# Optimization experiments

Measured on AMD Instinct MI355X. Metric: run time of the kernel, lower is better.

Reference implementation:

```python
import jax, jax.numpy as jnp
import numpy as np

N, E, F_IN, H = 50000, 800000, 500, 96

def setup_inputs() -> dict:
    key = jax.random.key(0)
    ks = jax.random.split(key, 10)
    x = jax.random.normal(ks[0], (N, F_IN), dtype=jnp.float32)
    src = jax.random.randint(ks[1], (E,), 0, N, dtype=jnp.int32)
    dst = jax.random.randint(ks[2], (E,), 0, N, dtype=jnp.int32)
    perm = jax.random.permutation(ks[3], N).astype(jnp.int32)
    W1 = jax.random.normal(ks[4], (F_IN, H), dtype=jnp.float32) / np.sqrt(F_IN)
    b1 = jnp.zeros((H,), jnp.float32)
    a1 = jnp.full((H,), 0.25, jnp.float32)  # PReLU init
    W2 = jax.random.normal(ks[5], (H, H), dtype=jnp.float32) / np.sqrt(H)
    b2 = jnp.zeros((H,), jnp.float32)
    a2 = jnp.full((H,), 0.25, jnp.float32)
    Wm = jax.random.normal(ks[6], (H, H), dtype=jnp.float32) / np.sqrt(H)
    bm = jnp.zeros((H,), jnp.float32)
    return {"x": x, "src": src, "dst": dst, "perm": perm,
            "W1": W1, "b1": b1, "a1": a1, "W2": W2, "b2": b2, "a2": a2,
            "Wm": Wm, "bm": bm}

def reference(x, src, dst, perm, W1, b1, a1, W2, b2, a2, Wm, bm):
    n = x.shape[0]
    ones = jnp.ones_like(src, dtype=x.dtype)
    deg_out = jnp.clip(jax.ops.segment_sum(ones, src, num_segments=n), 1.0)
    deg_in = jnp.clip(jax.ops.segment_sum(ones, dst, num_segments=n), 1.0)
    norm_out = (deg_out ** -0.5)[:, None]  # [N,1]
    norm_in = (deg_in ** -0.5)[:, None]

    def gconv(h, W, b, a):
        # DGL GraphConv, norm='both': D_out^-1/2 -> W -> A -> D_in^-1/2 -> +b -> PReLU
        h = (h * norm_out) @ W                                  # [N,H]
        agg = jax.ops.segment_sum(h[src], dst, num_segments=n)  # SpMM via gather/scatter
        h = agg * norm_in + b
        return jnp.where(h >= 0, h, a * h)                      # PReLU

    def encode(feat):
        h = gconv(feat, W1, b1, a1)
        return gconv(h, W2, b2, a2)

    z1 = encode(x)
    z2 = encode(x[perm])  # corrupted view: permuted node features
    z1 = z1 @ Wm + bm
    z2 = z2 @ Wm + bm
    return jnp.concatenate([z1.sum(1), z2.sum(1)], axis=0)  # [2N]
```

## Files before the change

### kernel.cpp

```cpp
#include <hip/hip_runtime.h>

#define H96 96

typedef __attribute__((ext_vector_type(8))) short bf16x8_t;
typedef __attribute__((ext_vector_type(4))) float f32x4_t;
typedef __attribute__((ext_vector_type(8))) _Float16 half8_t;

#define NRANGE 8
#define NCHUNK 64

__global__ __launch_bounds__(256) void hist2_kernel(const int* __restrict__ src,
                                                    const int* __restrict__ dst,
                                                    unsigned short* __restrict__ parts,
                                                    int E, int RS, int ecpc) {
    extern __shared__ int h[];
    int r = blockIdx.x >> 6;
    int c = blockIdx.x & 63;
    int lo = r * RS;
    for (int i = threadIdx.x; i < 2 * RS; i += 256) h[i] = 0;
    __syncthreads();
    int e0 = c * ecpc;
    int e1 = min(e0 + ecpc, E);
    for (int base = e0 + threadIdx.x * 4; base < e1; base += 1024) {
        int cnt = min(4, e1 - base);
        if (cnt == 4) {
            int4 sv = *(const int4*)(src + base);
            int4 dv = *(const int4*)(dst + base);
            int a;
            a = sv.x - lo; if ((unsigned)a < (unsigned)RS) atomicAdd(&h[a], 1);
            a = sv.y - lo; if ((unsigned)a < (unsigned)RS) atomicAdd(&h[a], 1);
            a = sv.z - lo; if ((unsigned)a < (unsigned)RS) atomicAdd(&h[a], 1);
            a = sv.w - lo; if ((unsigned)a < (unsigned)RS) atomicAdd(&h[a], 1);
            a = dv.x - lo; if ((unsigned)a < (unsigned)RS) atomicAdd(&h[RS + a], 1);
            a = dv.y - lo; if ((unsigned)a < (unsigned)RS) atomicAdd(&h[RS + a], 1);
            a = dv.z - lo; if ((unsigned)a < (unsigned)RS) atomicAdd(&h[RS + a], 1);
            a = dv.w - lo; if ((unsigned)a < (unsigned)RS) atomicAdd(&h[RS + a], 1);
        } else {
            for (int k = 0; k < cnt; k++) {
                int a = src[base + k] - lo;
                if ((unsigned)a < (unsigned)RS) atomicAdd(&h[a], 1);
                a = dst[base + k] - lo;
                if ((unsigned)a < (unsigned)RS) atomicAdd(&h[RS + a], 1);
            }
        }
    }
    __syncthreads();
    unsigned short* po = parts + ((size_t)(r * 2 + 0) * NCHUNK + c) * RS;
    unsigned short* pi = parts + ((size_t)(r * 2 + 1) * NCHUNK + c) * RS;
    for (int i = threadIdx.x; i < RS; i += 256) {
        po[i] = (unsigned short)h[i];
        pi[i] = (unsigned short)h[RS + i];
    }
}

__global__ void degred_kernel(const unsigned short* __restrict__ parts,
                              const int* __restrict__ perm,
                              int* __restrict__ deg_in, int* __restrict__ iperm,
                              float* __restrict__ no, float* __restrict__ ni,
                              int N, int RS) {
    int i = blockIdx.x * 256 + threadIdx.x;
    if (i >= N) return;
    int r = i / RS, idx = i - r * RS;
    const unsigned short* po = parts + ((size_t)(r * 2 + 0) * NCHUNK) * RS + idx;
    const unsigned short* pi = parts + ((size_t)(r * 2 + 1) * NCHUNK) * RS + idx;
    int so = 0, si = 0;
#pragma unroll
    for (int c = 0; c < NCHUNK; c++) {
        so += po[(size_t)c * RS];
        si += pi[(size_t)c * RS];
    }
    deg_in[i] = si;
    no[i] = rsqrtf(fmaxf((float)so, 1.0f));
    ni[i] = rsqrtf(fmaxf((float)si, 1.0f));
    iperm[perm[i]] = i;
}

__global__ void scanA_kernel(const int* __restrict__ in, int* __restrict__ pre,
                             int* __restrict__ bsums, int n) {
    __shared__ int s[256];
    int i = blockIdx.x * 256 + threadIdx.x;
    int v = (i < n) ? in[i] : 0;
    s[threadIdx.x] = v;
    __syncthreads();
    for (int off = 1; off < 256; off <<= 1) {
        int t = (threadIdx.x >= off) ? s[threadIdx.x - off] : 0;
        __syncthreads();
        s[threadIdx.x] += t;
        __syncthreads();
    }
    if (i < n) pre[i] = s[threadIdx.x] - v;
    if (threadIdx.x == 255) bsums[blockIdx.x] = s[255];
}

__global__ void scanB_kernel(int* __restrict__ bsums, int nb) {
    __shared__ int s[256];
    int v = (threadIdx.x < nb) ? bsums[threadIdx.x] : 0;
    s[threadIdx.x] = v;
    __syncthreads();
    for (int off = 1; off < 256; off <<= 1) {
        int t = (threadIdx.x >= off) ? s[threadIdx.x - off] : 0;
        __syncthreads();
        s[threadIdx.x] += t;
        __syncthreads();
    }
    if (threadIdx.x < nb) bsums[threadIdx.x] = s[threadIdx.x] - v;
}

__global__ void rowfin_kernel(const int* __restrict__ pre, const int* __restrict__ bsums,
                              int* __restrict__ row_start, int* __restrict__ cursor,
                              int N, int E) {
    int i = blockIdx.x * 256 + threadIdx.x;
    if (i < N) {
        int v = pre[i] + bsums[blockIdx.x];
        row_start[i] = v;
        cursor[i] = v;
    }
    if (i == 0) row_start[N] = E;
}

__global__ void scatter_kernel(const int* __restrict__ src, const int* __restrict__ dst,
                               const float* __restrict__ norm_out,
                               int* __restrict__ cursor, int2* __restrict__ edge2, int E) {
    int e = blockIdx.x * 256 + threadIdx.x;
    if (e < E) {
        int d = dst[e];
        int s = src[e];
        int p = atomicAdd(cursor + d, 1);
        edge2[p] = make_int2(s, __float_as_int(norm_out[s]));
    }
}

__global__ void histblk_kernel(const int* __restrict__ deg, int* __restrict__ hb,
                               int N, int nb) {
    __shared__ int h[256];
    h[threadIdx.x] = 0;
    __syncthreads();
    int i = blockIdx.x * 256 + threadIdx.x;
    if (i < N) atomicAdd(&h[min(deg[i], 255)], 1);
    __syncthreads();
    hb[threadIdx.x * nb + blockIdx.x] = h[threadIdx.x];
}

__global__ void place2_kernel(const int* __restrict__ deg, const int* __restrict__ hpre,
                              const int* __restrict__ bsums, int* __restrict__ order,
                              int N, int nb) {
    __shared__ int cur[256];
    int idx = threadIdx.x * nb + blockIdx.x;
    cur[threadIdx.x] = hpre[idx] + bsums[idx >> 8];
    __syncthreads();
    int i = blockIdx.x * 256 + threadIdx.x;
    if (i < N) {
        int b = min(deg[i], 255);
        int p = atomicAdd(&cur[b], 1);
        order[p] = i;
    }
}

__device__ __forceinline__ void f2bf2(float v, unsigned short& h, unsigned short& l) {
    unsigned int b = __float_as_uint(v);
    unsigned short hh = (unsigned short)((b + 0x7FFFu + ((b >> 16) & 1u)) >> 16);
    float fh = __uint_as_float(((unsigned int)hh) << 16);
    float r = v - fh;
    unsigned int rb = __float_as_uint(r);
    unsigned short ll = (unsigned short)((rb + 0x7FFFu + ((rb >> 16) & 1u)) >> 16);
    h = hh; l = ll;
}

__device__ __forceinline__ void cvt8(const float f[8], bf16x8_t& ah, bf16x8_t& al) {
    union { unsigned int u[4]; bf16x8_t v; } H, L;
#pragma unroll
    for (int i = 0; i < 4; i++) {
        float v0 = f[2 * i], v1 = f[2 * i + 1];
        unsigned int b0 = __float_as_uint(v0);
        unsigned int b1 = __float_as_uint(v1);
        unsigned int m0 = b0 & 0xFFFF0000u;
        unsigned int m1 = b1 & 0xFFFF0000u;
        float r0 = v0 - __uint_as_float(m0);
        float r1 = v1 - __uint_as_float(m1);
        H.u[i] = (b0 >> 16) | m1;
        L.u[i] = (__float_as_uint(r0) >> 16) | (__float_as_uint(r1) & 0xFFFF0000u);
    }
    ah = H.v; al = L.v;
}

__global__ void weights_prep(const float* __restrict__ W1, const float* __restrict__ W2,
                             const float* __restrict__ Wm, const float* __restrict__ bm,
                             unsigned short* __restrict__ w1h, unsigned short* __restrict__ w1l,
                             unsigned short* __restrict__ w2h, unsigned short* __restrict__ w2l,
                             float* __restrict__ wsum, float* __restrict__ bsum,
                             int F, int KP1) {
    int idx = blockIdx.x * 256 + threadIdx.x;
    int z1 = 96 * KP1, z2 = z1 + 96 * 96;
    if (idx < z1) {
        int n = idx / KP1, k = idx - n * KP1;
        float v = (k < F) ? W1[(size_t)k * 96 + n] : 0.f;
        unsigned short h, l;
        f2bf2(v, h, l);
        w1h[idx] = h; w1l[idx] = l;
    } else if (idx < z2) {
        int t = idx - z1;
        int n = t / 96, k = t - n * 96;
        float v = W2[(size_t)k * 96 + n];
        unsigned short h, l;
        f2bf2(v, h, l);
        w2h[t] = h; w2l[t] = l;
    } else if (idx < z2 + 96) {
        int c = idx - z2;
        float s = 0.f;
        for (int j = 0; j < 96; j++) s += Wm[c * 96 + j];
        wsum[c] = s;
    } else if (idx == z2 + 96) {
        float s = 0.f;
        for (int j = 0; j < 96; j++) s += bm[j];
        bsum[0] = s;
    }
}

#define GBM 64
#define GBK 32

__device__ __forceinline__ void gload_lds16(const void* g, void* l) {
    __builtin_amdgcn_global_load_lds(
        (const __attribute__((address_space(1))) unsigned int*)g,
        (__attribute__((address_space(3))) unsigned int*)l, 16, 0, 0);
}

__global__ __launch_bounds__(256, 6) void gemm_mfma(const void* __restrict__ Av,
                                                    const unsigned short* __restrict__ Bth,
                                                    const unsigned short* __restrict__ Btl,
                                                    _Float16* __restrict__ C16,
                                                    const int* __restrict__ ipermArr,
                                                    int M, int K, int KP) {
    __shared__ alignas(16) unsigned short Bs[2][2][96][4][8];
    int tid = threadIdx.x;
    int wid = tid >> 6, lane = tid & 63;
    int q = lane >> 4, mn = lane & 15;
    int row0 = blockIdx.x * GBM + wid * 16;
    int arow = min(row0 + mn, M - 1);
    int nk = (K + GBK - 1) / GBK;

    const float* A32 = (const float*)Av;

    const unsigned short* gsrc[3];
    int lbase[3];
#pragma unroll
    for (int i = 0; i < 3; i++) {
        int c = wid * 192 + i * 64 + lane;
        int part = (c >= 384) ? 1 : 0;
        int rem = c - part * 384;
        int row = rem >> 2, slot = rem & 3;
        int kc = slot ^ ((row >> 1) & 3);
        gsrc[i] = (part ? Btl : Bth) + (size_t)row * KP + kc * 8;
        lbase[i] = (wid * 192 + i * 64) * 8;
    }

    auto stage = [&](int t, int buf) {
#pragma unroll
        for (int i = 0; i < 3; i++)
            gload_lds16(gsrc[i] + (size_t)t * GBK, &Bs[buf][0][0][0][0] + lbase[i]);
    };

    auto loadA = [&](int t, float* f) {
        int gk = t * GBK + q * 8;
        if (gk + 8 <= K) {
            float4 v0 = *(const float4*)(A32 + (size_t)arow * K + gk);
            float4 v1 = *(const float4*)(A32 + (size_t)arow * K + gk + 4);
            f[0] = v0.x; f[1] = v0.y; f[2] = v0.z; f[3] = v0.w;
            f[4] = v1.x; f[5] = v1.y; f[6] = v1.z; f[7] = v1.w;
        } else {
#pragma unroll
            for (int c = 0; c < 8; c++)
                f[c] = (gk + c < K) ? A32[(size_t)arow * K + gk + c] : 0.f;
        }
    };

    f32x4_t acc[6] = {};
    float f[8], fn[8];

    stage(0, 0);
    loadA(0, f);

    int slotR = q ^ ((mn >> 1) & 3);

    for (int t = 0; t < nk; t++) {
        int tn = (t + 1 < nk) ? t + 1 : nk - 1;
        stage(tn, (t + 1) & 1);
        loadA(tn, fn);
        asm volatile("s_waitcnt vmcnt(5)" ::: "memory");
        __builtin_amdgcn_sched_barrier(0);
        __builtin_amdgcn_s_barrier();

        bf16x8_t ah, al;
        cvt8(f, ah, al);

        const unsigned short* bp = &Bs[t & 1][0][0][0][0] + mn * 32 + slotR * 8;
#pragma unroll
        for (int ct = 0; ct < 6; ct++) {
            bf16x8_t bh = *(const bf16x8_t*)(bp + ct * 512);
            bf16x8_t bl = *(const bf16x8_t*)(bp + 3072 + ct * 512);
            acc[ct] = __builtin_amdgcn_mfma_f32_16x16x32_bf16(ah, bh, acc[ct], 0, 0, 0);
            acc[ct] = __builtin_amdgcn_mfma_f32_16x16x32_bf16(ah, bl, acc[ct], 0, 0, 0);
            acc[ct] = __builtin_amdgcn_mfma_f32_16x16x32_bf16(al, bh, acc[ct], 0, 0, 0);
        }
        asm volatile("s_waitcnt lgkmcnt(0)" ::: "memory");
        __builtin_amdgcn_sched_barrier(0);
        __builtin_amdgcn_s_barrier();

#pragma unroll
        for (int c = 0; c < 8; c++) f[c] = fn[c];
    }

    asm volatile("s_waitcnt vmcnt(0)" ::: "memory");
    __builtin_amdgcn_sched_barrier(0);

#pragma unroll
    for (int reg = 0; reg < 4; reg++) {
        int gr = row0 + q * 4 + reg;
        if (gr < M) {
            int ip = ipermArr[gr];
#pragma unroll
            for (int ct = 0; ct < 6; ct++) {
                _Float16 v = (_Float16)acc[ct][reg];
                C16[(size_t)gr * 192 + ct * 16 + mn] = v;
                C16[(size_t)ip * 192 + 96 + ct * 16 + mn] = v;
            }
        }
    }
}

__global__ __launch_bounds__(256, 4) void gemm_small(const _Float16* __restrict__ A16,
                                                     const unsigned short* __restrict__ Bth,
                                                     const unsigned short* __restrict__ Btl,
                                                     _Float16* __restrict__ C16,
                                                     int M) {
    __shared__ alignas(16) unsigned short Bs[3][2][96][4][8];
    const int K = 96;
    int tid = threadIdx.x;
    int wid = tid >> 6, lane = tid & 63;
    int q = lane >> 4, mn = lane & 15;
    int row0 = blockIdx.x * GBM + wid * 16;
    int arow = min(row0 + mn, M - 1);

    const unsigned short* gsrc[3];
    int lbase[3];
#pragma unroll
    for (int i = 0; i < 3; i++) {
        int c = wid * 192 + i * 64 + lane;
        int part = (c >= 384) ? 1 : 0;
        int rem = c - part * 384;
        int row = rem >> 2, slot = rem & 3;
        int kc = slot ^ ((row >> 1) & 3);
        gsrc[i] = (part ? Btl : Bth) + (size_t)row * K + kc * 8;
        lbase[i] = (wid * 192 + i * 64) * 8;
    }

#pragma unroll
    for (int t = 0; t < 3; t++)
#pragma unroll
        for (int i = 0; i < 3; i++)
            gload_lds16(gsrc[i] + (size_t)t * GBK, &Bs[t][0][0][0][0] + lbase[i]);

    uint4 ra0 = *(const uint4*)(A16 + (size_t)arow * K + 0 * GBK + q * 8);
    uint4 ra1 = *(const uint4*)(A16 + (size_t)arow * K + 1 * GBK + q * 8);
    uint4 ra2 = *(const uint4*)(A16 + (size_t)arow * K + 2 * GBK + q * 8);

    asm volatile("s_waitcnt vmcnt(0)" ::: "memory");
    __builtin_amdgcn_sched_barrier(0);
    __builtin_amdgcn_s_barrier();

    f32x4_t acc[6] = {};
    int slotR = q ^ ((mn >> 1) & 3);

    auto step = [&](int t, const uint4& raw) {
        float f[8];
        const _Float16* hp = (const _Float16*)&raw;
#pragma unroll
        for (int c = 0; c < 8; c++) f[c] = (float)hp[c];
        bf16x8_t ah, al;
        cvt8(f, ah, al);
        const unsigned short* bp = &Bs[t][0][0][0][0] + mn * 32 + slotR * 8;
#pragma unroll
        for (int ct = 0; ct < 6; ct++) {
            bf16x8_t bh = *(const bf16x8_t*)(bp + ct * 512);
            bf16x8_t bl = *(const bf16x8_t*)(bp + 3072 + ct * 512);
            acc[ct] = __builtin_amdgcn_mfma_f32_16x16x32_bf16(ah, bh, acc[ct], 0, 0, 0);
            acc[ct] = __builtin_amdgcn_mfma_f32_16x16x32_bf16(ah, bl, acc[ct], 0, 0, 0);
            acc[ct] = __builtin_amdgcn_mfma_f32_16x16x32_bf16(al, bh, acc[ct], 0, 0, 0);
        }
    };

    step(0, ra0);
    step(1, ra1);
    step(2, ra2);

#pragma unroll
    for (int reg = 0; reg < 4; reg++) {
        int gr = row0 + q * 4 + reg;
        if (gr < M) {
#pragma unroll
            for (int ct = 0; ct < 6; ct++)
                C16[(size_t)gr * H96 + ct * 16 + mn] = (_Float16)acc[ct][reg];
        }
    }
}

__device__ __forceinline__ void fmah8(float4& a, float4& b, float s, half8_t v) {
    a.x = fmaf(s, (float)v[0], a.x); a.y = fmaf(s, (float)v[1], a.y);
    a.z = fmaf(s, (float)v[2], a.z); a.w = fmaf(s, (float)v[3], a.w);
    b.x = fmaf(s, (float)v[4], b.x); b.y = fmaf(s, (float)v[5], b.y);
    b.z = fmaf(s, (float)v[6], b.z); b.w = fmaf(s, (float)v[7], b.w);
}

__device__ __forceinline__ float4 prelu4(float4 acc, float ni, float4 b, float4 a) {
    float4 h;
    h.x = fmaf(acc.x, ni, b.x); h.x = (h.x >= 0.f) ? h.x : a.x * h.x;
    h.y = fmaf(acc.y, ni, b.y); h.y = (h.y >= 0.f) ? h.y : a.y * h.y;
    h.z = fmaf(acc.z, ni, b.z); h.z = (h.z >= 0.f) ? h.z : a.z * h.z;
    h.w = fmaf(acc.w, ni, b.w); h.w = (h.w >= 0.f) ? h.w : a.w * h.w;
    return h;
}

__global__ __launch_bounds__(384) void spmm1_dual(
        const half8_t* __restrict__ yp, const int* __restrict__ row_start,
        const int2* __restrict__ edge2, const int* __restrict__ order,
        const float* __restrict__ norm_out, const float* __restrict__ norm_in,
        const float* __restrict__ b1, const float* __restrict__ a1,
        half8_t* __restrict__ hpair, int N) {
    int g = blockIdx.x * 32 + threadIdx.y;
    if (g >= N) return;
    int d = order[g];
    int tx = threadIdx.x;
    int beg = row_start[d], end = row_start[d + 1];
    const half8_t* yt = yp + tx;
    float4 a1a = {0,0,0,0}, a1b = {0,0,0,0}, a2a = {0,0,0,0}, a2b = {0,0,0,0};
    int j = beg;
    for (; j + 8 <= end; j += 8) {
        int2 e[8];
#pragma unroll
        for (int q = 0; q < 8; q++) e[q] = edge2[j + q];
        half8_t u[8], w[8];
#pragma unroll
        for (int q = 0; q < 8; q++) u[q] = yt[(size_t)e[q].x * 24];
#pragma unroll
        for (int q = 0; q < 8; q++) w[q] = yt[(size_t)e[q].x * 24 + 12];
#pragma unroll
        for (int q = 0; q < 8; q++) {
            float n = __int_as_float(e[q].y);
            fmah8(a1a, a1b, n, u[q]);
            fmah8(a2a, a2b, n, w[q]);
        }
    }
    for (; j < end; j++) {
        int2 e = edge2[j];
        float n = __int_as_float(e.y);
        fmah8(a1a, a1b, n, yt[(size_t)e.x * 24]);
        fmah8(a2a, a2b, n, yt[(size_t)e.x * 24 + 12]);
    }
    float ni = norm_in[d], no = norm_out[d];
    float4 bb0 = ((const float4*)b1)[tx * 2], bb1 = ((const float4*)b1)[tx * 2 + 1];
    float4 aa0 = ((const float4*)a1)[tx * 2], aa1 = ((const float4*)a1)[tx * 2 + 1];
    float4 r1a = prelu4(a1a, ni, bb0, aa0), r1b = prelu4(a1b, ni, bb1, aa1);
    float4 r2a = prelu4(a2a, ni, bb0, aa0), r2b = prelu4(a2b, ni, bb1, aa1);
    half8_t o1, o2;
    o1[0] = (_Float16)(r1a.x * no); o1[1] = (_Float16)(r1a.y * no);
    o1[2] = (_Float16)(r1a.z * no); o1[3] = (_Float16)(r1a.w * no);
    o1[4] = (_Float16)(r1b.x * no); o1[5] = (_Float16)(r1b.y * no);
    o1[6] = (_Float16)(r1b.z * no); o1[7] = (_Float16)(r1b.w * no);
    o2[0] = (_Float16)(r2a.x * no); o2[1] = (_Float16)(r2a.y * no);
    o2[2] = (_Float16)(r2a.z * no); o2[3] = (_Float16)(r2a.w * no);
    o2[4] = (_Float16)(r2b.x * no); o2[5] = (_Float16)(r2b.y * no);
    o2[6] = (_Float16)(r2b.z * no); o2[7] = (_Float16)(r2b.w * no);
    hpair[(size_t)d * 24 + tx] = o1;
    hpair[(size_t)d * 24 + 12 + tx] = o2;
}

__global__ __launch_bounds__(384) void spmm2_dual(
        const half8_t* __restrict__ th,
        const int* __restrict__ row_start, const int2* __restrict__ edge2,
        const int* __restrict__ order, const float* __restrict__ norm_in,
        const float* __restrict__ b2, const float* __restrict__ a2,
        const float* __restrict__ wsum, const float* __restrict__ bsum,
        float* __restrict__ outp, int N) {
    int g = blockIdx.x * 32 + threadIdx.y;
    int tx = threadIdx.x;
    int ty = threadIdx.y;
    bool valid = (g < N);
    int d = valid ? order[g] : 0;
    int beg = 0, end = 0;
    if (valid) { beg = row_start[d]; end = row_start[d + 1]; }
    const half8_t* t1 = th + tx;
    float4 a1a = {0,0,0,0}, a1b = {0,0,0,0}, a2a = {0,0,0,0}, a2b = {0,0,0,0};
    int j = beg;
    for (; j + 8 <= end; j += 8) {
        int s[8];
#pragma unroll
        for (int q = 0; q < 8; q++) s[q] = edge2[j + q].x;
        half8_t u[8], w[8];
#pragma unroll
        for (int q = 0; q < 8; q++) u[q] = t1[(size_t)s[q] * 24];
#pragma unroll
        for (int q = 0; q < 8; q++) w[q] = t1[(size_t)s[q] * 24 + 12];
#pragma unroll
        for (int q = 0; q < 8; q++) {
            fmah8(a1a, a1b, 1.f, u[q]);
            fmah8(a2a, a2b, 1.f, w[q]);
        }
    }
    for (; j < end; j++) {
        int s = edge2[j].x;
        fmah8(a1a, a1b, 1.f, t1[(size_t)s * 24]);
        fmah8(a2a, a2b, 1.f, t1[(size_t)s * 24 + 12]);
    }
    float ni = valid ? norm_in[d] : 0.f;
    float4 bb0 = ((const float4*)b2)[tx * 2], bb1 = ((const float4*)b2)[tx * 2 + 1];
    float4 aa0 = ((const float4*)a2)[tx * 2], aa1 = ((const float4*)a2)[tx * 2 + 1];
    float4 wv0 = ((const float4*)wsum)[tx * 2], wv1 = ((const float4*)wsum)[tx * 2 + 1];
    float4 r1a = prelu4(a1a, ni, bb0, aa0), r1b = prelu4(a1b, ni, bb1, aa1);
    float4 r2a = prelu4(a2a, ni, bb0, aa0), r2b = prelu4(a2b, ni, bb1, aa1);
    float p1 = r1a.x * wv0.x + r1a.y * wv0.y + r1a.z * wv0.z + r1a.w * wv0.w
             + r1b.x * wv1.x + r1b.y * wv1.y + r1b.z * wv1.z + r1b.w * wv1.w;
    float p2 = r2a.x * wv0.x + r2a.y * wv0.y + r2a.z * wv0.z + r2a.w * wv0.w
             + r2b.x * wv1.x + r2b.y * wv1.y + r2b.z * wv1.z + r2b.w * wv1.w;
    __shared__ float red1[32][12];
    __shared__ float red2[32][12];
    red1[ty][tx] = p1;
    red2[ty][tx] = p2;
    __syncthreads();
    if (tx == 0 && valid) {
        float s1 = 0.f, s2 = 0.f;
#pragma unroll
        for (int k = 0; k < 12; k++) { s1 += red1[ty][k]; s2 += red2[ty][k]; }
        outp[d] = s1 + bsum[0];
        outp[N + d] = s2 + bsum[0];
    }
}

extern "C" void kernel_launch(void* const* d_in, const int* in_sizes, int n_in,
                              void* d_out, int out_size, void* d_ws, size_t ws_size,
                              hipStream_t stream) {
    const float* x    = (const float*)d_in[0];
    const int*   src  = (const int*)d_in[1];
    const int*   dst  = (const int*)d_in[2];
    const int*   perm = (const int*)d_in[3];
    const float* W1   = (const float*)d_in[4];
    const float* b1   = (const float*)d_in[5];
    const float* a1   = (const float*)d_in[6];
    const float* W2   = (const float*)d_in[7];
    const float* b2   = (const float*)d_in[8];
    const float* a2   = (const float*)d_in[9];
    const float* Wm   = (const float*)d_in[10];
    const float* bm   = (const float*)d_in[11];
    float* out = (float*)d_out;

    int E = in_sizes[1];
    int N = in_sizes[3];
    int F = in_sizes[0] / N;
    int KP1 = ((F + GBK - 1) / GBK) * GBK;

    size_t NP = ((size_t)N + 256) & ~(size_t)255;
    size_t EP = ((size_t)E + 255) & ~(size_t)255;
    int nb = (N + 255) / 256;
    size_t HB = ((size_t)256 * nb + 255) & ~(size_t)255;

    int* iperm     = (int*)d_ws;
    int* deg_in    = iperm + NP;
    int* pre       = deg_in + NP;
    int* row_start = pre + NP;
    int* cursor    = row_start + NP;
    int* order     = cursor + NP;
    int* bsums     = order + NP;
    int* hb        = bsums + 256;
    int* hpre      = hb + HB;
    int2* edge2    = (int2*)(hpre + HB);
    float* norm_out = (float*)(edge2 + EP);
    float* norm_in  = norm_out + NP;
    float* wsum     = norm_in + NP;
    float* bsum     = wsum + 128;
    unsigned short* w1th = (unsigned short*)(bsum + 128);
    unsigned short* w1tl = w1th + 49664;
    unsigned short* w2th = w1tl + 49664;
    unsigned short* w2tl = w2th + 9728;
    _Float16* fpA = (_Float16*)(w2tl + 9728);
    _Float16* fpB = fpA + ((size_t)N * 192 + 256);
    _Float16* ypair = fpA;
    _Float16* hpair = fpB;
    _Float16* th    = fpA;

    unsigned short* parts = (unsigned short*)fpA;

    int RS = (N + NRANGE - 1) / NRANGE;
    int ecpc = ((E + NCHUNK - 1) / NCHUNK + 3) & ~3;
    hist2_kernel<<<NRANGE * NCHUNK, 256, 2 * RS * (int)sizeof(int), stream>>>(
        src, dst, parts, E, RS, ecpc);
    degred_kernel<<<(N + 255) / 256, 256, 0, stream>>>(parts, perm, deg_in, iperm,
                                                       norm_out, norm_in, N, RS);

    scanA_kernel<<<nb, 256, 0, stream>>>(deg_in, pre, bsums, N);
    scanB_kernel<<<1, 256, 0, stream>>>(bsums, nb);
    rowfin_kernel<<<nb, 256, 0, stream>>>(pre, bsums, row_start, cursor, N, E);
    scatter_kernel<<<(E + 255) / 256, 256, 0, stream>>>(src, dst, norm_out, cursor,
                                                        edge2, E);

    histblk_kernel<<<nb, 256, 0, stream>>>(deg_in, hb, N, nb);
    int n2 = 256 * nb;
    int nb2 = (n2 + 255) / 256;
    scanA_kernel<<<nb2, 256, 0, stream>>>(hb, hpre, bsums, n2);
    scanB_kernel<<<1, 256, 0, stream>>>(bsums, nb2);
    place2_kernel<<<nb, 256, 0, stream>>>(deg_in, hpre, bsums, order, N, nb);

    int wtot = 96 * KP1 + 96 * 96 + 96 + 1;
    weights_prep<<<(wtot + 255) / 256, 256, 0, stream>>>(W1, W2, Wm, bm, w1th, w1tl,
                                                         w2th, w2tl, wsum, bsum, F, KP1);

    gemm_mfma<<<(N + GBM - 1) / GBM, 256, 0, stream>>>(x, w1th, w1tl, ypair, iperm,
                                                       N, F, KP1);

    int nsb = (N + 31) / 32;
    spmm1_dual<<<nsb, dim3(12, 32), 0, stream>>>(
        (const half8_t*)ypair, row_start, edge2, order, norm_out, norm_in,
        b1, a1, (half8_t*)hpair, N);

    gemm_small<<<(2 * N + GBM - 1) / GBM, 256, 0, stream>>>(hpair, w2th, w2tl, th, 2 * N);

    spmm2_dual<<<nsb, dim3(12, 32), 0, stream>>>(
        (const half8_t*)th, row_start, edge2, order, norm_in, b2, a2,
        wsum, bsum, out, N);
}
```

Before: 389.1 us.

## Scatter edges via per-chunk LDS cursors and split GEMM1 columns across waves

```diff
diff --git a/kernel.cpp b/kernel.cpp
--- a/kernel.cpp
+++ b/kernel.cpp
@@ -75,6 +75,21 @@
     iperm[perm[i]] = i;
 }
 
+__global__ void chunkpre_kernel(const unsigned short* __restrict__ parts,
+                                const int* __restrict__ row_start,
+                                int* __restrict__ cpre, int N, int RS) {
+    int i = blockIdx.x * 256 + threadIdx.x;
+    if (i >= N) return;
+    int r = i / RS, idx = i - r * RS;
+    const unsigned short* pi = parts + ((size_t)(r * 2 + 1) * NCHUNK) * RS + idx;
+    int run = row_start[i];
+#pragma unroll
+    for (int c = 0; c < NCHUNK; c++) {
+        cpre[(size_t)c * N + i] = run;
+        run += pi[(size_t)c * RS];
+    }
+}
+
 __global__ void scanA_kernel(const int* __restrict__ in, int* __restrict__ pre,
                              int* __restrict__ bsums, int n) {
     __shared__ int s[256];
@@ -107,26 +122,33 @@
 }
 
 __global__ void rowfin_kernel(const int* __restrict__ pre, const int* __restrict__ bsums,
-                              int* __restrict__ row_start, int* __restrict__ cursor,
-                              int N, int E) {
+                              int* __restrict__ row_start, int N, int E) {
     int i = blockIdx.x * 256 + threadIdx.x;
-    if (i < N) {
-        int v = pre[i] + bsums[blockIdx.x];
-        row_start[i] = v;
-        cursor[i] = v;
-    }
+    if (i < N) row_start[i] = pre[i] + bsums[blockIdx.x];
     if (i == 0) row_start[N] = E;
 }
 
-__global__ void scatter_kernel(const int* __restrict__ src, const int* __restrict__ dst,
-                               const float* __restrict__ norm_out,
-                               int* __restrict__ cursor, int2* __restrict__ edge2, int E) {
-    int e = blockIdx.x * 256 + threadIdx.x;
-    if (e < E) {
-        int d = dst[e];
-        int s = src[e];
-        int p = atomicAdd(cursor + d, 1);
-        edge2[p] = make_int2(s, __float_as_int(norm_out[s]));
+__global__ __launch_bounds__(256) void scatter8_kernel(const int* __restrict__ src,
+                                                       const int* __restrict__ dst,
+                                                       const float* __restrict__ norm_out,
+                                                       const int* __restrict__ cpre,
+                                                       int2* __restrict__ edge2,
+                                                       int E, int N, int RS, int ecpc) {
+    extern __shared__ int cur[];
+    int r = blockIdx.x >> 6, c = blockIdx.x & 63;
+    int lo = r * RS;
+    int len = min(RS, N - lo);
+    for (int i = threadIdx.x; i < len; i += 256)
+        cur[i] = cpre[(size_t)c * N + lo + i];
+    __syncthreads();
+    int e0 = c * ecpc, e1 = min(e0 + ecpc, E);
+    for (int e = e0 + threadIdx.x; e < e1; e += 256) {
+        int d = dst[e] - lo;
+        if ((unsigned)d < (unsigned)len) {
+            int s = src[e];
+            int p = atomicAdd(&cur[d], 1);
+            edge2[p] = make_int2(s, __float_as_int(norm_out[s]));
+        }
     }
 }
 
@@ -216,7 +238,6 @@
     }
 }
 
-#define GBM 64
 #define GBK 32
 
 __device__ __forceinline__ void gload_lds16(const void* g, void* l) {
@@ -235,7 +256,8 @@
     int tid = threadIdx.x;
     int wid = tid >> 6, lane = tid & 63;
     int q = lane >> 4, mn = lane & 15;
-    int row0 = blockIdx.x * GBM + wid * 16;
+    int rg = wid >> 1, ch = wid & 1;
+    int row0 = blockIdx.x * 32 + rg * 16;
     int arow = min(row0 + mn, M - 1);
     int nk = (K + GBK - 1) / GBK;
 
@@ -274,7 +296,7 @@
         }
     };
 
-    f32x4_t acc[6] = {};
+    f32x4_t acc[3] = {};
     float f[8], fn[8];
 
     stage(0, 0);
@@ -293,14 +315,14 @@
         bf16x8_t ah, al;
         cvt8(f, ah, al);
 
-        const unsigned short* bp = &Bs[t & 1][0][0][0][0] + mn * 32 + slotR * 8;
-#pragma unroll
-        for (int ct = 0; ct < 6; ct++) {
-            bf16x8_t bh = *(const bf16x8_t*)(bp + ct * 512);
-            bf16x8_t bl = *(const bf16x8_t*)(bp + 3072 + ct * 512);
-            acc[ct] = __builtin_amdgcn_mfma_f32_16x16x32_bf16(ah, bh, acc[ct], 0, 0, 0);
-            acc[ct] = __builtin_amdgcn_mfma_f32_16x16x32_bf16(ah, bl, acc[ct], 0, 0, 0);
-            acc[ct] = __builtin_amdgcn_mfma_f32_16x16x32_bf16(al, bh, acc[ct], 0, 0, 0);
+        const unsigned short* bp = &Bs[t & 1][0][0][0][0] + mn * 32 + slotR * 8 + ch * 1536;
+#pragma unroll
+        for (int ct2 = 0; ct2 < 3; ct2++) {
+            bf16x8_t bh = *(const bf16x8_t*)(bp + ct2 * 512);
+            bf16x8_t bl = *(const bf16x8_t*)(bp + 3072 + ct2 * 512);
+            acc[ct2] = __builtin_amdgcn_mfma_f32_16x16x32_bf16(ah, bh, acc[ct2], 0, 0, 0);
+            acc[ct2] = __builtin_amdgcn_mfma_f32_16x16x32_bf16(ah, bl, acc[ct2], 0, 0, 0);
+            acc[ct2] = __builtin_amdgcn_mfma_f32_16x16x32_bf16(al, bh, acc[ct2], 0, 0, 0);
         }
         asm volatile("s_waitcnt lgkmcnt(0)" ::: "memory");
         __builtin_amdgcn_sched_barrier(0);
@@ -319,10 +341,11 @@
         if (gr < M) {
             int ip = ipermArr[gr];
 #pragma unroll
-            for (int ct = 0; ct < 6; ct++) {
-                _Float16 v = (_Float16)acc[ct][reg];
-                C16[(size_t)gr * 192 + ct * 16 + mn] = v;
-                C16[(size_t)ip * 192 + 96 + ct * 16 + mn] = v;
+            for (int ct2 = 0; ct2 < 3; ct2++) {
+                int col = (ch * 3 + ct2) * 16 + mn;
+                _Float16 v = (_Float16)acc[ct2][reg];
+                C16[(size_t)gr * 192 + col] = v;
+                C16[(size_t)ip * 192 + 96 + col] = v;
             }
         }
     }
@@ -338,7 +361,7 @@
     int tid = threadIdx.x;
     int wid = tid >> 6, lane = tid & 63;
     int q = lane >> 4, mn = lane & 15;
-    int row0 = blockIdx.x * GBM + wid * 16;
+    int row0 = blockIdx.x * 64 + wid * 16;
     int arow = min(row0 + mn, M - 1);
 
     const unsigned short* gsrc[3];
@@ -587,6 +610,7 @@
     _Float16* th    = fpA;
 
     unsigned short* parts = (unsigned short*)fpA;
+    int* cpre = (int*)fpB;
 
     int RS = (N + NRANGE - 1) / NRANGE;
     int ecpc = ((E + NCHUNK - 1) / NCHUNK + 3) & ~3;
@@ -597,9 +621,10 @@
 
     scanA_kernel<<<nb, 256, 0, stream>>>(deg_in, pre, bsums, N);
     scanB_kernel<<<1, 256, 0, stream>>>(bsums, nb);
-    rowfin_kernel<<<nb, 256, 0, stream>>>(pre, bsums, row_start, cursor, N, E);
-    scatter_kernel<<<(E + 255) / 256, 256, 0, stream>>>(src, dst, norm_out, cursor,
-                                                        edge2, E);
+    rowfin_kernel<<<nb, 256, 0, stream>>>(pre, bsums, row_start, N, E);
+    chunkpre_kernel<<<(N + 255) / 256, 256, 0, stream>>>(parts, row_start, cpre, N, RS);
+    scatter8_kernel<<<NRANGE * NCHUNK, 256, RS * (int)sizeof(int), stream>>>(
+        src, dst, norm_out, cpre, edge2, E, N, RS, ecpc);
 
     histblk_kernel<<<nb, 256, 0, stream>>>(deg_in, hb, N, nb);
     int n2 = 256 * nb;
@@ -612,15 +637,15 @@
     weights_prep<<<(wtot + 255) / 256, 256, 0, stream>>>(W1, W2, Wm, bm, w1th, w1tl,
                                                          w2th, w2tl, wsum, bsum, F, KP1);
 
-    gemm_mfma<<<(N + GBM - 1) / GBM, 256, 0, stream>>>(x, w1th, w1tl, ypair, iperm,
-                                                       N, F, KP1);
+    gemm_mfma<<<(N + 31) / 32, 256, 0, stream>>>(x, w1th, w1tl, ypair, iperm,
+                                                 N, F, KP1);
 
     int nsb = (N + 31) / 32;
     spmm1_dual<<<nsb, dim3(12, 32), 0, stream>>>(
         (const half8_t*)ypair, row_start, edge2, order, norm_out, norm_in,
         b1, a1, (half8_t*)hpair, N);
 
-    gemm_small<<<(2 * N + GBM - 1) / GBM, 256, 0, stream>>>(hpair, w2th, w2tl, th, 2 * N);
+    gemm_small<<<(2 * N + 63) / 64, 256, 0, stream>>>(hpair, w2th, w2tl, th, 2 * N);
 
     spmm2_dual<<<nsb, dim3(12, 32), 0, stream>>>(
         (const half8_t*)th, row_start, edge2, order, norm_in, b2, a2,
```

After: 405.0 us. 1.04x slower.
